# Performance work log

Hardware: AMD Instinct MI355X
Metric: run time of the kernel (lower is better)

## Reference

```python
import jax, jax.numpy as jnp
import numpy as np

H = 512; VT = 10000; VN = 1000; ET = 256; EN = 256
A = 50; B = 8; L = 128; SOS = 0


def setup_inputs():
    key = jax.random.key(0)
    ks = jax.random.split(key, 12)
    g = lambda k, s: jax.random.normal(k, s, jnp.float32) * 0.02
    inp = {}
    inp["n_tensor"] = jax.random.randint(ks[0], (B, L), 0, VN)
    inp["t_tensor"] = jax.random.randint(ks[1], (B, L), 0, VT)
    inp["p_tensor"] = jax.random.randint(ks[2], (B, L), 0, L)
    # embedding tables; padding rows (padding_idx) zeroed as nn.Embedding init does
    inp["embN"] = g(ks[3], (VN, EN)).at[VN - 1].set(0.0)
    inp["embT"] = g(ks[4], (VT + A + 3, ET)).at[VT - 1].set(0.0)
    inp["W_hid"] = g(ks[5], (H, H)); inp["b_hid"] = jnp.zeros((H,), jnp.float32)
    inp["W_mem"] = g(ks[6], (H, H)); inp["b_mem"] = jnp.zeros((H,), jnp.float32)
    inp["v_w"] = g(ks[7], (H,)); inp["v_b"] = jnp.zeros((), jnp.float32)
    inp["W_ih"] = g(ks[8], (4 * H, EN + ET)); inp["W_hh"] = g(ks[9], (4 * H, H))
    inp["b_ih"] = jnp.zeros((4 * H,), jnp.float32); inp["b_hh"] = jnp.zeros((4 * H,), jnp.float32)
    inp["W_g"] = g(ks[10], (3 * H, VT + 3)); inp["b_g"] = jnp.zeros((VT + 3,), jnp.float32)
    inp["W_s"] = g(ks[11], (2 * H,)); inp["b_s"] = jnp.zeros((), jnp.float32)
    return inp


def _forward(embN, embT, W_hid, b_hid, W_mem, b_mem, v_w, v_b,
             W_ih, W_hh, b_ih, b_hh, W_g, b_g, W_s, b_s,
             n_tensor, t_tensor, p_tensor):
    full_mask = (n_tensor == VN - 1)                      # [B, L] eof mask
    sos = jnp.full((B, 1), SOS, n_tensor.dtype)
    n_in = jnp.concatenate([sos, n_tensor[:, :-1]], 1)    # teacher-forced inputs
    t_in = jnp.concatenate([sos, t_tensor[:, :-1]], 1)
    par = jnp.concatenate([jnp.zeros((B, 1), p_tensor.dtype), p_tensor[:, :-1]], 1)
    hs0 = jnp.zeros((B, L, H), jnp.float32)               # growing memory buffer
    h0 = jnp.zeros((B, H), jnp.float32)
    c0 = jnp.zeros((B, H), jnp.float32)
    barange = jnp.arange(B)
    arangeA = jnp.arange(A)

    def step(carry, xs):
        hs, h, c = carry
        t, n_t, t_t, p_t, tgt = xs
        # embedding gathers + single-layer LSTM cell (torch gate order i,f,g,o)
        x = jnp.concatenate([embN[n_t], embT[t_t]], 1)    # [B, EN+ET]
        gates = x @ W_ih.T + h @ W_hh.T + (b_ih + b_hh)
        i, f, gg, o = jnp.split(gates, 4, axis=1)
        c = jax.nn.sigmoid(f) * c + jax.nn.sigmoid(i) * jnp.tanh(gg)
        h = jax.nn.sigmoid(o) * jnp.tanh(c)
        # sliding-window memory hs[:, max(t-A,0):t], fixed-size slice + validity mask
        s = jnp.maximum(t - A, 0)
        mem = jax.lax.dynamic_slice(hs, (0, s, 0), (B, A, H))   # [B, A, H]
        fm = jax.lax.dynamic_slice(full_mask, (0, s), (B, A))   # [B, A]
        valid = (s + arangeA) < t                               # [A] positions already written
        mask = fm | ~valid[None, :]
        # additive attention: v^T tanh(W_hid h + W_mem mem)
        sc = jnp.tanh((h @ W_hid.T + b_hid)[:, None, :] + mem @ W_mem.T + b_mem)
        sc = sc @ v_w + v_b                                     # [B, A]
        sc = jnp.where(mask, -1e20, sc)
        attn = jax.nn.softmax(sc, axis=1)
        context = jnp.einsum('ba,bah->bh', attn, mem)
        h_parent = hs[barange, p_t]                             # per-batch gather on memory
        wt = jax.nn.log_softmax(jnp.concatenate([context, h, h_parent], 1) @ W_g + b_g, axis=1)
        log_attn = jax.nn.log_softmax(sc, axis=1)
        st = jax.nn.log_sigmoid(jnp.concatenate([context, h], 1) @ W_s + b_s)[:, None]  # [B,1]
        out = jnp.concatenate(
            [st + wt, jnp.log(jnp.clip(-jnp.expm1(st), 1e-18, 1e18)) + log_attn], 1)    # [B, VT+3+A]
        hs = hs.at[:, t].set(h)                                 # scatter new hidden into buffer
        loss_t = -jnp.take_along_axis(out, tgt[:, None], axis=1)[:, 0]  # NLLLoss(reduction='none')
        pred = jnp.argmax(out, axis=1)
        return (hs, h, c), (loss_t, pred)

    ts = jnp.arange(L)
    _, (losses, preds) = jax.lax.scan(
        step, (hs0, h0, c0), (ts, n_in.T, t_in.T, par.T, t_tensor.T))
    return losses.sum(), preds.T


def reference(n_tensor, t_tensor, p_tensor, embN, embT, W_hid, b_hid, W_mem, b_mem,
              v_w, v_b, W_ih, W_hh, b_ih, b_hh, W_g, b_g, W_s, b_s):
    return _forward(embN, embT, W_hid, b_hid, W_mem, b_mem, v_w, v_b,
                    W_ih, W_hh, b_ih, b_hh, W_g, b_g, W_s, b_s,
                    n_tensor, t_tensor, p_tensor)
```

## Files before the change

kernel.cpp:

```cpp
#include <hip/hip_runtime.h>
#include <hip/hip_bf16.h>
#include <math.h>

#define H_ 512
#define VN_ 1000
#define NG_ 10003
#define NGP_ 10240
#define NCHUNK 80
#define A_ 50
#define B_ 8
#define L_ 128
#define R_ 1024

typedef __hip_bfloat16 bf16;
typedef __attribute__((ext_vector_type(8))) short bf16x8;
typedef __attribute__((ext_vector_type(4))) float f32x4;

typedef union { unsigned long long u[2]; bf16x8 v; } frag_u;

__device__ __forceinline__ float fsig(float x) { return 1.0f / (1.0f + __expf(-x)); }
__device__ __forceinline__ float ftanh(float x) { return 1.0f - 2.0f / (1.0f + __expf(2.0f * x)); }

__device__ __forceinline__ short b16(float v) {
    __hip_bfloat16 h = __float2bfloat16(v);
    return *(short*)&h;
}

__device__ __forceinline__ unsigned long long ald(const unsigned long long* p) {
    return __hip_atomic_load(p, __ATOMIC_RELAXED, __HIP_MEMORY_SCOPE_AGENT);
}
__device__ __forceinline__ int aldi(const int* p) {
    return __hip_atomic_load(p, __ATOMIC_RELAXED, __HIP_MEMORY_SCOPE_AGENT);
}
__device__ __forceinline__ void ast32(unsigned int* p, unsigned int v) {
    __hip_atomic_store(p, v, __ATOMIC_RELAXED, __HIP_MEMORY_SCOPE_AGENT);
}
__device__ __forceinline__ void asti(int* p, int v) {
    __hip_atomic_store(p, v, __ATOMIC_RELAXED, __HIP_MEMORY_SCOPE_AGENT);
}

__global__ void k_prep(int* flags, float* bkq,
                       const float* __restrict__ bmem, const float* __restrict__ bhid,
                       float* out,
                       const float* __restrict__ Wih, bf16* __restrict__ wihb,
                       const int* __restrict__ nt, const int* __restrict__ tt,
                       const float* __restrict__ embN, const float* __restrict__ embT,
                       bf16* __restrict__ X)
{
    const int i = blockIdx.x * 256 + threadIdx.x;
    const int total = gridDim.x * 256;
    if (i < 32)
        __hip_atomic_store(&flags[i], 0, __ATOMIC_RELAXED, __HIP_MEMORY_SCOPE_AGENT);
    if (i < 1024) bkq[i] = (i < 512) ? bmem[i] : bhid[i - 512];
    if (i == 0) out[0] = 0.f;
    for (int j = i; j < 2048 * 512; j += total)
        wihb[j] = __float2bfloat16(Wih[j]);
    {
        int r = i >> 9, k = i & 511;
        int t = r >> 3, b = r & 7;
        float v;
        if (k < 256) {
            int id = (t == 0) ? 0 : nt[b * L_ + t - 1];
            v = embN[id * 256 + k];
        } else {
            int id = (t == 0) ? 0 : tt[b * L_ + t - 1];
            v = embT[id * 256 + (k - 256)];
        }
        X[i] = __float2bfloat16(v);
    }
}

#define LSTM_BLOCKS 16
#define XTRA 240

#define DECLW(i) bf16x8 Wa##i, Wb##i;
#define LOADW(i) { \
    float4 a0 = *(const float4*)(wr0 + (i)*32); \
    float4 a1 = *(const float4*)(wr0 + (i)*32 + 4); \
    float4 c0 = *(const float4*)(wr1 + (i)*32); \
    float4 c1 = *(const float4*)(wr1 + (i)*32 + 4); \
    Wa##i[0]=b16(a0.x); Wa##i[1]=b16(a0.y); Wa##i[2]=b16(a0.z); Wa##i[3]=b16(a0.w); \
    Wa##i[4]=b16(a1.x); Wa##i[5]=b16(a1.y); Wa##i[6]=b16(a1.z); Wa##i[7]=b16(a1.w); \
    Wb##i[0]=b16(c0.x); Wb##i[1]=b16(c0.y); Wb##i[2]=b16(c0.z); Wb##i[3]=b16(c0.w); \
    Wb##i[4]=b16(c1.x); Wb##i[5]=b16(c1.y); Wb##i[6]=b16(c1.z); Wb##i[7]=b16(c1.w); }
#define LDF(i) frag_u fu##i; fu##i.u[0] = ald(src + (i)*128); fu##i.u[1] = ald(src + (i)*128 + 1);
#define MM(i) \
    acc0 = __builtin_amdgcn_mfma_f32_16x16x32_bf16(Wa##i, fu##i.v, acc0, 0, 0, 0); \
    acc1 = __builtin_amdgcn_mfma_f32_16x16x32_bf16(Wb##i, fu##i.v, acc1, 0, 0, 0);

__launch_bounds__(256, 1)
__global__ void k_lstm(const float* __restrict__ Whh, const float* __restrict__ xg,
                       bf16* __restrict__ hsb,
                       unsigned long long* __restrict__ bfr, int* __restrict__ flags,
                       const float* __restrict__ Wg, bf16* __restrict__ WT,
                       const float* __restrict__ Wmem, const float* __restrict__ Whid,
                       bf16* __restrict__ wkq)
{
    __shared__ float gl[4][32][9];
    __shared__ short S[64][65];
    const int tid  = threadIdx.x;
    const int x    = blockIdx.x;

    if (x >= LSTM_BLOCKS) {
        for (int i = (x - LSTM_BLOCKS) * 256 + tid; i < 2 * 512 * 512; i += XTRA * 256) {
            float v = (i < 512 * 512) ? Wmem[i] : Whid[i - 512 * 512];
            wkq[i] = __float2bfloat16(v);
        }
        const int c = tid & 63;
        const int r0 = (tid >> 6) * 16;
        const int n_l = tid >> 2;
        const int kq = (tid & 3) * 16;
        for (int tile = x - LSTM_BLOCKS; tile < 160 * 24; tile += XTRA) {
            int n0 = (tile % 160) * 64, k0 = (tile / 160) * 64;
            __syncthreads();
            #pragma unroll
            for (int i = 0; i < 16; ++i) {
                int k = r0 + i;
                int n = n0 + c;
                float v = (n < NG_) ? Wg[(size_t)(k0 + k) * NG_ + n] : 0.f;
                S[c][k] = b16(v);
            }
            __syncthreads();
            bf16* dst = WT + (size_t)(n0 + n_l) * 1536 + k0 + kq;
            #pragma unroll
            for (int j = 0; j < 2; ++j) {
                bf16x8 v;
                #pragma unroll
                for (int e = 0; e < 8; ++e) v[e] = S[n_l][kq + j * 8 + e];
                *(bf16x8*)(dst + j * 8) = v;
            }
        }
        return;
    }

    const int lane = tid & 63;
    const int w    = tid >> 6;
    const int m_l  = lane & 15;
    const int kg   = lane >> 4;
    const int n    = lane & 15;
    unsigned int* bfr32 = (unsigned int*)bfr;

    const float* wr0 = Whh + (size_t)(w * 512 + x * 32 + m_l) * 512 + kg * 8;
    const float* wr1 = wr0 + (size_t)16 * 512;
    DECLW(0)  DECLW(1)  DECLW(2)  DECLW(3)  DECLW(4)  DECLW(5)  DECLW(6)  DECLW(7)
    DECLW(8)  DECLW(9)  DECLW(10) DECLW(11) DECLW(12) DECLW(13) DECLW(14) DECLW(15)
    LOADW(0)  LOADW(1)  LOADW(2)  LOADW(3)  LOADW(4)  LOADW(5)  LOADW(6)  LOADW(7)
    LOADW(8)  LOADW(9)  LOADW(10) LOADW(11) LOADW(12) LOADW(13) LOADW(14) LOADW(15)
    asm volatile("" : "+v"(Wa0), "+v"(Wb0), "+v"(Wa1), "+v"(Wb1), "+v"(Wa2), "+v"(Wb2),
                      "+v"(Wa3), "+v"(Wb3), "+v"(Wa4), "+v"(Wb4), "+v"(Wa5), "+v"(Wb5),
                      "+v"(Wa6), "+v"(Wb6), "+v"(Wa7), "+v"(Wb7));
    asm volatile("" : "+v"(Wa8), "+v"(Wb8), "+v"(Wa9), "+v"(Wb9), "+v"(Wa10), "+v"(Wb10),
                      "+v"(Wa11), "+v"(Wb11), "+v"(Wa12), "+v"(Wb12), "+v"(Wa13), "+v"(Wb13),
                      "+v"(Wa14), "+v"(Wb14), "+v"(Wa15), "+v"(Wb15));

    const int u_l = tid >> 3;
    const int b   = tid & 7;
    float creg = 0.f;
    int fearly = 0;

    for (int t = 0; t < L_; ++t) {
        const float* xr = xg + ((size_t)t * B_ + b) * 2048 + x * 32 + u_l;
        float xi = xr[0], xf = xr[512], xgg = xr[1024], xo = xr[1536];

        f32x4 acc0 = {0.f, 0.f, 0.f, 0.f};
        f32x4 acc1 = {0.f, 0.f, 0.f, 0.f};
        if (t > 0) {
            if (!__all(fearly >= t)) {
                for (;;) {
                    int v = (lane < LSTM_BLOCKS) ? aldi(&flags[lane]) : t;
                    if (__all(v >= t)) break;
                    __builtin_amdgcn_s_sleep(1);
                }
            }
            const unsigned long long* src =
                bfr + (size_t)((t + 1) & 1) * 2048 + lane * 2;
            LDF(0)  LDF(1)  LDF(2)  LDF(3)  LDF(4)  LDF(5)  LDF(6)  LDF(7)
            LDF(8)  LDF(9)  LDF(10) LDF(11) LDF(12) LDF(13) LDF(14) LDF(15)
            __builtin_amdgcn_sched_barrier(0);
            MM(0)  MM(1)  MM(2)  MM(3)  MM(4)  MM(5)  MM(6)  MM(7)
            MM(8)  MM(9)  MM(10) MM(11) MM(12) MM(13) MM(14) MM(15)
        }
        if (n < 8) {
            #pragma unroll
            for (int i = 0; i < 4; ++i) {
                gl[w][kg * 4 + i][n]      = acc0[i];
                gl[w][16 + kg * 4 + i][n] = acc1[i];
            }
        }
        __syncthreads();
        float gi = gl[0][u_l][b] + xi;
        float gf = gl[1][u_l][b] + xf;
        float gg = gl[2][u_l][b] + xgg;
        float go = gl[3][u_l][b] + xo;
        float iv = fsig(gi), fv = fsig(gf), gv = ftanh(gg), ov = fsig(go);
        creg = fv * creg + iv * gv;
        float h = ov * ftanh(creg);
        float h2 = __shfl_xor(h, 8);
        unsigned pay = 0;
        if ((u_l & 1) == 0) {
            pay = (unsigned)(unsigned short)b16(h)
                | ((unsigned)(unsigned short)b16(h2) << 16);
            int q = u_l >> 3, p = (u_l & 7) >> 1;
            ast32(bfr32 + (size_t)(t & 1) * 4096 + x * 256 + (b + 16 * q) * 4 + p, pay);
        }
        fearly = (lane < LSTM_BLOCKS && lane != x) ? aldi(&flags[lane]) : 0x7FFFFFFF;
        asm volatile("s_waitcnt vmcnt(0)" ::: "memory");
        __syncthreads();
        if (tid == 0)
            asti(&flags[x], t + 1);
        if ((u_l & 1) == 0)
            *(unsigned int*)(hsb + (size_t)(t * B_ + b) * 512 + x * 32 + u_l) = pay;
    }
}

__launch_bounds__(256)
__global__ void k_attn(const bf16* __restrict__ hsb, const float* __restrict__ kmq,
                       const float* __restrict__ vw,
                       const float* __restrict__ vb, const int* __restrict__ nt,
                       const int* __restrict__ pt, const float* __restrict__ Wsv,
                       const float* __restrict__ bs, bf16* __restrict__ gcat,
                       float* __restrict__ logattn, float* __restrict__ stbuf)
{
    const int r = blockIdx.x;
    const int t = r >> 3, b = r & 7;
    const int tid = threadIdx.x;
    const int lane = tid & 63, wave = tid >> 6;
    int s = t - A_; if (s < 0) s = 0;
    __shared__ float qv[512];
    __shared__ float vwl[512];
    __shared__ float sc[A_];
    __shared__ float attn[A_];
    __shared__ float red[4];
    for (int i = tid; i < 512; i += 256) {
        qv[i] = kmq[(size_t)r * 1024 + 512 + i];
        vwl[i] = vw[i];
    }
    __syncthreads();
    for (int a = wave; a < A_; a += 4) {
        int pos = s + a;
        float v = -1e20f;
        bool masked = (pos >= t) || (nt[b * L_ + pos] == VN_ - 1);
        if (!masked) {
            const float* kr = kmq + (size_t)(pos * B_ + b) * 1024;
            float p = 0.f;
            for (int k = lane; k < 512; k += 64)
                p += vwl[k] * ftanh(qv[k] + kr[k]);
            for (int off = 32; off; off >>= 1) p += __shfl_down(p, off);
            v = p + vb[0];
        }
        if (lane == 0) sc[a] = v;
    }
    __syncthreads();
    if (tid < 64) {
        float v = (tid < A_) ? sc[tid] : -INFINITY;
        float m = v;
        for (int off = 32; off; off >>= 1) m = fmaxf(m, __shfl_xor(m, off));
        float e = (tid < A_) ? expf(v - m) : 0.f;
        float d = e;
        for (int off = 32; off; off >>= 1) d += __shfl_xor(d, off);
        if (tid < A_) {
            attn[tid] = e / d;
            logattn[(size_t)r * A_ + tid] = (v - m) - logf(d);
        }
    }
    __syncthreads();
    const int k0 = tid * 2;
    float c0 = 0.f, c1 = 0.f;
    for (int a = 0; a < A_; ++a) {
        int pos = s + a;
        if (pos >= t) break;
        float w = attn[a];
        unsigned u = *(const unsigned*)((const unsigned short*)hsb + (size_t)(pos * B_ + b) * 512 + k0);
        c0 += w * __uint_as_float(u << 16);
        c1 += w * __uint_as_float(u & 0xffff0000u);
    }
    unsigned ucur = *(const unsigned*)((const unsigned short*)hsb + (size_t)(t * B_ + b) * 512 + k0);
    int par = (t == 0) ? 0 : pt[b * L_ + t - 1];
    unsigned upar = 0;
    if (par < t)
        upar = *(const unsigned*)((const unsigned short*)hsb + (size_t)(par * B_ + b) * 512 + k0);
    float hx = __uint_as_float(ucur << 16), hy = __uint_as_float(ucur & 0xffff0000u);
    bf16* g = gcat + (size_t)r * 1536;
    g[k0]     = __float2bfloat16(c0);
    g[k0 + 1] = __float2bfloat16(c1);
    *(unsigned*)(g + 512 + k0)  = ucur;
    *(unsigned*)(g + 1024 + k0) = upar;
    float part = c0 * Wsv[k0] + c1 * Wsv[k0 + 1]
               + hx * Wsv[512 + k0] + hy * Wsv[512 + k0 + 1];
    for (int off = 32; off; off >>= 1) part += __shfl_down(part, off);
    if (lane == 0) red[wave] = part;
    __syncthreads();
    if (tid == 0) {
        float z = red[0] + red[1] + red[2] + red[3] + bs[0];
        stbuf[r] = -log1pf(expf(-z));
    }
}

__launch_bounds__(256, 2)
__global__ void k_gemm128b(const bf16* __restrict__ Ag, const bf16* __restrict__ Bg,
                           const float* __restrict__ b1, const float* __restrict__ b2,
                           float* __restrict__ C, int N, int K)
{
    __shared__ short As[128 * 32];
    __shared__ short Bs[128 * 32];
    const int tid = threadIdx.x;
    const int lane = tid & 63, wave = tid >> 6;
    const int wr = wave >> 1, wc = wave & 1;
    const int m0 = blockIdx.y * 128, n0 = blockIdx.x * 128;
    f32x4 acc[4][4] = {};
    for (int k0 = 0; k0 < K; k0 += 32) {
        __syncthreads();
        #pragma unroll
        for (int h = 0; h < 2; ++h) {
            int o = tid + h * 256;
            int row = o >> 2;
            int kc = (o & 3) ^ (row & 3);
            const bf16* ga = Ag + (size_t)(m0 + row) * K + k0 + kc * 8;
            const bf16* gb = Bg + (size_t)(n0 + row) * K + k0 + kc * 8;
            unsigned ldso = h * 4096 + wave * 1024;
            __builtin_amdgcn_global_load_lds(
                (const __attribute__((address_space(1))) void*)ga,
                (__attribute__((address_space(3))) void*)((char*)As + ldso), 16, 0, 0);
            __builtin_amdgcn_global_load_lds(
                (const __attribute__((address_space(1))) void*)gb,
                (__attribute__((address_space(3))) void*)((char*)Bs + ldso), 16, 0, 0);
        }
        asm volatile("s_waitcnt vmcnt(0)" ::: "memory");
        __syncthreads();
        bf16x8 af[4], bf[4];
        #pragma unroll
        for (int mi = 0; mi < 4; ++mi) {
            int ra = wr * 64 + mi * 16 + (lane & 15);
            af[mi] = *(const bf16x8*)&As[ra * 32 + (((lane >> 4) ^ (ra & 3)) * 8)];
        }
        #pragma unroll
        for (int ni = 0; ni < 4; ++ni) {
            int rb = wc * 64 + ni * 16 + (lane & 15);
            bf[ni] = *(const bf16x8*)&Bs[rb * 32 + (((lane >> 4) ^ (rb & 3)) * 8)];
        }
        #pragma unroll
        for (int mi = 0; mi < 4; ++mi)
            #pragma unroll
            for (int ni = 0; ni < 4; ++ni)
                acc[mi][ni] = __builtin_amdgcn_mfma_f32_16x16x32_bf16(af[mi], bf[ni], acc[mi][ni], 0, 0, 0);
    }
    const int col = lane & 15, rq = (lane >> 4) * 4;
    #pragma unroll
    for (int mi = 0; mi < 4; ++mi)
        #pragma unroll
        for (int ni = 0; ni < 4; ++ni) {
            int nn = n0 + wc * 64 + ni * 16 + col;
            float bias = (b1 ? b1[nn] : 0.f) + (b2 ? b2[nn] : 0.f);
            #pragma unroll
            for (int i = 0; i < 4; ++i)
                C[(size_t)(m0 + wr * 64 + mi * 16 + rq + i) * N + nn] = acc[mi][ni][i] + bias;
        }
}

__launch_bounds__(256, 2)
__global__ void k_gemm128p(const bf16* __restrict__ Ag, const bf16* __restrict__ Bg,
                           const float* __restrict__ bg, const int* __restrict__ tt,
                           float* __restrict__ pst)
{
    __shared__ short As[128 * 32];
    __shared__ short Bs[128 * 32];
    __shared__ float bgl[128];
    __shared__ float mrg[128][6];
    const int tid = threadIdx.x;
    const int lane = tid & 63, wave = tid >> 6;
    const int wr = wave >> 1, wc = wave & 1;
    const int col16 = lane & 15, rq = (lane >> 4) * 4;
    const int chunk = blockIdx.x;
    const int m0 = blockIdx.y * 128;
    const int n0 = chunk * 128;
    const int K = 1536;

    if (tid < 128) bgl[tid] = (n0 + tid < NG_) ? bg[n0 + tid] : -INFINITY;

    float M[4][4], S[4][4], AV[4][4], TGT[4][4]; int AI[4][4]; int tgt[4][4];
    #pragma unroll
    for (int mi = 0; mi < 4; ++mi)
        #pragma unroll
        for (int i = 0; i < 4; ++i) {
            M[mi][i] = -INFINITY; S[mi][i] = 0.f; AV[mi][i] = -INFINITY;
            TGT[mi][i] = -INFINITY; AI[mi][i] = 0x7FFFFFFF;
            int row = m0 + wr * 64 + mi * 16 + rq + i;
            tgt[mi][i] = tt[(row & 7) * L_ + (row >> 3)];
        }

    f32x4 acc[4][4] = {};
    for (int k0 = 0; k0 < K; k0 += 32) {
        __syncthreads();
        #pragma unroll
        for (int h = 0; h < 2; ++h) {
            int o = tid + h * 256;
            int row = o >> 2;
            int kc = (o & 3) ^ (row & 3);
            const bf16* ga = Ag + (size_t)(m0 + row) * K + k0 + kc * 8;
            const bf16* gb = Bg + (size_t)(n0 + row) * K + k0 + kc * 8;
            unsigned ldso = h * 4096 + wave * 1024;
            __builtin_amdgcn_global_load_lds(
                (const __attribute__((address_space(1))) void*)ga,
                (__attribute__((address_space(3))) void*)((char*)As + ldso), 16, 0, 0);
            __builtin_amdgcn_global_load_lds(
                (const __attribute__((address_space(1))) void*)gb,
                (__attribute__((address_space(3))) void*)((char*)Bs + ldso), 16, 0, 0);
        }
        asm volatile("s_waitcnt vmcnt(0)" ::: "memory");
        __syncthreads();
        bf16x8 af[4], bf[4];
        #pragma unroll
        for (int mi = 0; mi < 4; ++mi) {
            int ra = wr * 64 + mi * 16 + col16;
            af[mi] = *(const bf16x8*)&As[ra * 32 + (((lane >> 4) ^ (ra & 3)) * 8)];
        }
        #pragma unroll
        for (int ni = 0; ni < 4; ++ni) {
            int rb = wc * 64 + ni * 16 + col16;
            bf[ni] = *(const bf16x8*)&Bs[rb * 32 + (((lane >> 4) ^ (rb & 3)) * 8)];
        }
        #pragma unroll
        for (int mi = 0; mi < 4; ++mi)
            #pragma unroll
            for (int ni = 0; ni < 4; ++ni)
                acc[mi][ni] = __builtin_amdgcn_mfma_f32_16x16x32_bf16(af[mi], bf[ni], acc[mi][ni], 0, 0, 0);
    }
    #pragma unroll
    for (int mi = 0; mi < 4; ++mi)
        #pragma unroll
        for (int i = 0; i < 4; ++i) {
            float v[4]; int nn[4];
            #pragma unroll
            for (int ni = 0; ni < 4; ++ni) {
                int cl = wc * 64 + ni * 16 + col16;
                v[ni] = acc[mi][ni][i] + bgl[cl];
                nn[ni] = n0 + cl;
            }
            float lv = v[0]; int li = nn[0];
            #pragma unroll
            for (int ni = 1; ni < 4; ++ni)
                if (v[ni] > lv) { lv = v[ni]; li = nn[ni]; }
            #pragma unroll
            for (int off = 1; off < 16; off <<= 1) {
                float ov = __shfl_xor(lv, off); int oi = __shfl_xor(li, off);
                if (ov > lv || (ov == lv && oi < li)) { lv = ov; li = oi; }
            }
            float nM = lv;
            float add = 0.f;
            if (nM != -INFINITY) {
                #pragma unroll
                for (int ni = 0; ni < 4; ++ni) add += expf(v[ni] - nM);
                #pragma unroll
                for (int off = 1; off < 16; off <<= 1) add += __shfl_xor(add, off);
            }
            M[mi][i] = nM; S[mi][i] = add;
            AV[mi][i] = lv; AI[mi][i] = li;
            float tv = -INFINITY;
            #pragma unroll
            for (int ni = 0; ni < 4; ++ni)
                if (nn[ni] == tgt[mi][i]) tv = v[ni];
            #pragma unroll
            for (int off = 1; off < 16; off <<= 1)
                tv = fmaxf(tv, __shfl_xor(tv, off));
            TGT[mi][i] = tv;
        }
    __syncthreads();
    if (wc == 1 && col16 == 0) {
        #pragma unroll
        for (int mi = 0; mi < 4; ++mi)
            #pragma unroll
            for (int i = 0; i < 4; ++i) {
                int rl = wr * 64 + mi * 16 + rq + i;
                mrg[rl][0] = M[mi][i]; mrg[rl][1] = S[mi][i];
                mrg[rl][2] = AV[mi][i]; mrg[rl][3] = __int_as_float(AI[mi][i]);
                mrg[rl][4] = TGT[mi][i];
            }
    }
    __syncthreads();
    if (wc == 0 && col16 == 0) {
        #pragma unroll
        for (int mi = 0; mi < 4; ++mi)
            #pragma unroll
            for (int i = 0; i < 4; ++i) {
                int rl = wr * 64 + mi * 16 + rq + i;
                float oM = mrg[rl][0], oS = mrg[rl][1], oAV = mrg[rl][2];
                int oAI = __float_as_int(mrg[rl][3]);
                float oT = mrg[rl][4];
                float nM = fmaxf(M[mi][i], oM);
                float s1 = (S[mi][i] > 0.f) ? S[mi][i] * expf(M[mi][i] - nM) : 0.f;
                float s2 = (oS > 0.f) ? oS * expf(oM - nM) : 0.f;
                float av = AV[mi][i]; int ai = AI[mi][i];
                if (oAV > av || (oAV == av && oAI < ai)) { av = oAV; ai = oAI; }
                float* p = pst + ((size_t)chunk * R_ + (m0 + rl)) * 8;
                p[0] = nM; p[1] = s1 + s2; p[2] = av;
                p[3] = __int_as_float(ai); p[4] = fmaxf(TGT[mi][i], oT);
            }
    }
}

__launch_bounds__(64)
__global__ void k_loss2(const float* __restrict__ pst, const float* __restrict__ logattn,
                        const float* __restrict__ stbuf, float* __restrict__ out)
{
    const int r = blockIdx.x;
    const int lane = threadIdx.x;
    float M = -INFINITY, S = 0.f, AV = -INFINITY, TGT = -INFINITY;
    int AI = 0x7FFFFFFF;
    for (int c = lane; c < NCHUNK; c += 64) {
        const float* p = pst + ((size_t)c * R_ + r) * 8;
        float oM = p[0], oS = p[1], oAV = p[2];
        int oAI = __float_as_int(p[3]);
        float oT = p[4];
        float nM = fmaxf(M, oM);
        float s1 = (S > 0.f) ? S * expf(M - nM) : 0.f;
        float s2 = (oS > 0.f) ? oS * expf(oM - nM) : 0.f;
        M = nM; S = s1 + s2;
        if (oAV > AV || (oAV == AV && oAI < AI)) { AV = oAV; AI = oAI; }
        TGT = fmaxf(TGT, oT);
    }
    for (int off = 32; off; off >>= 1) {
        float oM = __shfl_xor(M, off), oS = __shfl_xor(S, off);
        float oAV = __shfl_xor(AV, off), oT = __shfl_xor(TGT, off);
        int oAI = __shfl_xor(AI, off);
        float nM = fmaxf(M, oM);
        float s1 = (S > 0.f) ? S * expf(M - nM) : 0.f;
        float s2 = (oS > 0.f) ? oS * expf(oM - nM) : 0.f;
        M = nM; S = s1 + s2;
        if (oAV > AV || (oAV == AV && oAI < AI)) { AV = oAV; AI = oAI; }
        TGT = fmaxf(TGT, oT);
    }
    if (lane == 0) {
        float lse = M + logf(S);
        float st = stbuf[r];
        const float* la = logattn + (size_t)r * A_;
        float lamax = la[0]; int aidx = 0;
        for (int a = 1; a < A_; ++a) if (la[a] > lamax) { lamax = la[a]; aidx = a; }
        float e1 = -expm1f(st);
        e1 = fminf(fmaxf(e1, 1e-18f), 1e18f);
        float lm = logf(e1);
        float p1 = st + M - lse;
        float p2 = lm + lamax;
        int pred = (p1 >= p2) ? AI : (NG_ + aidx);
        float loss = -(st + TGT - lse);
        atomicAdd(&out[0], loss);
        int t = r >> 3, b = r & 7;
        out[1 + b * L_ + t] = (float)pred;
    }
}

extern "C" void kernel_launch(void* const* d_in, const int* in_sizes, int n_in,
                              void* d_out, int out_size, void* d_ws, size_t ws_size,
                              hipStream_t stream)
{
    (void)in_sizes; (void)n_in; (void)out_size; (void)ws_size;
    const int*   nt    = (const int*)d_in[0];
    const int*   tt    = (const int*)d_in[1];
    const int*   pt    = (const int*)d_in[2];
    const float* embN  = (const float*)d_in[3];
    const float* embT  = (const float*)d_in[4];
    const float* W_hid = (const float*)d_in[5];
    const float* b_hid = (const float*)d_in[6];
    const float* W_mem = (const float*)d_in[7];
    const float* b_mem = (const float*)d_in[8];
    const float* v_w   = (const float*)d_in[9];
    const float* v_b   = (const float*)d_in[10];
    const float* W_ih  = (const float*)d_in[11];
    const float* W_hh  = (const float*)d_in[12];
    const float* b_ih  = (const float*)d_in[13];
    const float* b_hh  = (const float*)d_in[14];
    const float* W_g   = (const float*)d_in[15];
    const float* b_g   = (const float*)d_in[16];
    const float* W_s   = (const float*)d_in[17];
    const float* b_s   = (const float*)d_in[18];
    float* out = (float*)d_out;

    char* ws = (char*)d_ws;
    size_t o = 0;
    bf16*  WGT  = (bf16*)(ws + o);  o += (size_t)NGP_ * 1536 * 2;
    float* XG   = (float*)(ws + o); o += (size_t)R_ * 2048 * 4;
    bf16*  HSB  = (bf16*)(ws + o);  o += (size_t)R_ * H_ * 2;
    float* KMQ  = (float*)(ws + o); o += (size_t)R_ * 1024 * 4;
    bf16*  WKQ  = (bf16*)(ws + o);  o += (size_t)1024 * 512 * 2;
    float* BKQ  = (float*)(ws + o); o += (size_t)1024 * 4;
    bf16*  XB   = (bf16*)(ws + o);  o += (size_t)R_ * H_ * 2;
    bf16*  WIHB = (bf16*)(ws + o);  o += (size_t)2048 * 512 * 2;
    bf16*  GC   = (bf16*)(ws + o);  o += (size_t)R_ * 1536 * 2;
    float* LA   = (float*)(ws + o); o += (size_t)R_ * A_ * 4;
    float* ST   = (float*)(ws + o); o += (size_t)R_ * 4;
    float* PST  = (float*)(ws + o); o += (size_t)NCHUNK * R_ * 8 * 4;
    unsigned long long* BFR = (unsigned long long*)(ws + o); o += (size_t)4096 * 8;
    int*   FLG  = (int*)(ws + o);   o += 256;

    k_prep<<<2048, 256, 0, stream>>>(FLG, BKQ, b_mem, b_hid, out,
                                     W_ih, WIHB, nt, tt, embN, embT, XB);
    k_gemm128b<<<dim3(2048 / 128, R_ / 128), 256, 0, stream>>>(XB, WIHB, b_ih, b_hh, XG, 2048, 512);
    k_lstm<<<LSTM_BLOCKS + XTRA, 256, 0, stream>>>(W_hh, XG, HSB, BFR, FLG,
                                                   W_g, WGT, W_mem, W_hid, WKQ);
    k_gemm128b<<<dim3(1024 / 128, R_ / 128), 256, 0, stream>>>(HSB, WKQ, BKQ, nullptr, KMQ, 1024, 512);
    k_attn<<<R_, 256, 0, stream>>>(HSB, KMQ, v_w, v_b, nt, pt, W_s, b_s, GC, LA, ST);
    k_gemm128p<<<dim3(NCHUNK, R_ / 128), 256, 0, stream>>>(GC, WGT, b_g, tt, PST);
    k_loss2<<<R_, 64, 0, stream>>>(PST, LA, ST, out);
}
```

Before: 563.4 us.

## Fuse input-projection GEMM into LSTM kernel with per-chunk readiness flags

Removes the separate x@W_ih GEMM launch and computes it inside the persistent LSTM kernel's extra blocks. Each 128-row chunk publishes a completion counter, so the recurrent blocks can start once the first chunk is ready and wait only when they reach a later chunk. The MFMA accumulation over K is also split into two independent accumulator chains to shorten the dependency chain. This adds flag polling and atomic loads of XG, and it gives the weight-conversion work in those blocks less throughput.

```diff
diff --git a/kernel.cpp b/kernel.cpp
--- a/kernel.cpp
+++ b/kernel.cpp
@@ -32,10 +32,16 @@
 __device__ __forceinline__ int aldi(const int* p) {
     return __hip_atomic_load(p, __ATOMIC_RELAXED, __HIP_MEMORY_SCOPE_AGENT);
 }
+__device__ __forceinline__ float aldf(const float* p) {
+    return __hip_atomic_load(p, __ATOMIC_RELAXED, __HIP_MEMORY_SCOPE_AGENT);
+}
 __device__ __forceinline__ void ast32(unsigned int* p, unsigned int v) {
     __hip_atomic_store(p, v, __ATOMIC_RELAXED, __HIP_MEMORY_SCOPE_AGENT);
 }
 __device__ __forceinline__ void asti(int* p, int v) {
+    __hip_atomic_store(p, v, __ATOMIC_RELAXED, __HIP_MEMORY_SCOPE_AGENT);
+}
+__device__ __forceinline__ void astf(float* p, float v) {
     __hip_atomic_store(p, v, __ATOMIC_RELAXED, __HIP_MEMORY_SCOPE_AGENT);
 }
 
@@ -84,25 +90,94 @@
     Wb##i[0]=b16(c0.x); Wb##i[1]=b16(c0.y); Wb##i[2]=b16(c0.z); Wb##i[3]=b16(c0.w); \
     Wb##i[4]=b16(c1.x); Wb##i[5]=b16(c1.y); Wb##i[6]=b16(c1.z); Wb##i[7]=b16(c1.w); }
 #define LDF(i) frag_u fu##i; fu##i.u[0] = ald(src + (i)*128); fu##i.u[1] = ald(src + (i)*128 + 1);
-#define MM(i) \
-    acc0 = __builtin_amdgcn_mfma_f32_16x16x32_bf16(Wa##i, fu##i.v, acc0, 0, 0, 0); \
-    acc1 = __builtin_amdgcn_mfma_f32_16x16x32_bf16(Wb##i, fu##i.v, acc1, 0, 0, 0);
+#define MMa(i) \
+    acc0a = __builtin_amdgcn_mfma_f32_16x16x32_bf16(Wa##i, fu##i.v, acc0a, 0, 0, 0); \
+    acc1a = __builtin_amdgcn_mfma_f32_16x16x32_bf16(Wb##i, fu##i.v, acc1a, 0, 0, 0);
+#define MMb(i) \
+    acc0b = __builtin_amdgcn_mfma_f32_16x16x32_bf16(Wa##i, fu##i.v, acc0b, 0, 0, 0); \
+    acc1b = __builtin_amdgcn_mfma_f32_16x16x32_bf16(Wb##i, fu##i.v, acc1b, 0, 0, 0);
 
 __launch_bounds__(256, 1)
-__global__ void k_lstm(const float* __restrict__ Whh, const float* __restrict__ xg,
+__global__ void k_lstm(const float* __restrict__ Whh, float* __restrict__ xg,
                        bf16* __restrict__ hsb,
                        unsigned long long* __restrict__ bfr, int* __restrict__ flags,
                        const float* __restrict__ Wg, bf16* __restrict__ WT,
                        const float* __restrict__ Wmem, const float* __restrict__ Whid,
-                       bf16* __restrict__ wkq)
+                       bf16* __restrict__ wkq,
+                       const bf16* __restrict__ xb, const bf16* __restrict__ wihb,
+                       const float* __restrict__ bih, const float* __restrict__ bhh)
 {
     __shared__ float gl[4][32][9];
     __shared__ short S[64][65];
+    __shared__ short As[128 * 32];
+    __shared__ short Bs[128 * 32];
     const int tid  = threadIdx.x;
     const int x    = blockIdx.x;
+    const int lane = tid & 63;
+    const int wave = tid >> 6;
 
     if (x >= LSTM_BLOCKS) {
-        for (int i = (x - LSTM_BLOCKS) * 256 + tid; i < 2 * 512 * 512; i += XTRA * 256) {
+        const int d = x - LSTM_BLOCKS;
+        if (d < 128) {
+            const int m0 = (d >> 4) * 128, n0g = (d & 15) * 128;
+            const int wr = wave >> 1, wc = wave & 1;
+            const int K = 512;
+            f32x4 acc[4][4] = {};
+            for (int k0 = 0; k0 < K; k0 += 32) {
+                __syncthreads();
+                #pragma unroll
+                for (int h = 0; h < 2; ++h) {
+                    int o = tid + h * 256;
+                    int row = o >> 2;
+                    int kc = (o & 3) ^ (row & 3);
+                    const bf16* ga = xb + (size_t)(m0 + row) * K + k0 + kc * 8;
+                    const bf16* gb = wihb + (size_t)(n0g + row) * K + k0 + kc * 8;
+                    unsigned ldso = h * 4096 + wave * 1024;
+                    __builtin_amdgcn_global_load_lds(
+                        (const __attribute__((address_space(1))) void*)ga,
+                        (__attribute__((address_space(3))) void*)((char*)As + ldso), 16, 0, 0);
+                    __builtin_amdgcn_global_load_lds(
+                        (const __attribute__((address_space(1))) void*)gb,
+                        (__attribute__((address_space(3))) void*)((char*)Bs + ldso), 16, 0, 0);
+                }
+                asm volatile("s_waitcnt vmcnt(0)" ::: "memory");
+                __syncthreads();
+                bf16x8 af[4], bfv[4];
+                #pragma unroll
+                for (int mi = 0; mi < 4; ++mi) {
+                    int ra = wr * 64 + mi * 16 + (lane & 15);
+                    af[mi] = *(const bf16x8*)&As[ra * 32 + (((lane >> 4) ^ (ra & 3)) * 8)];
+                }
+                #pragma unroll
+                for (int ni = 0; ni < 4; ++ni) {
+                    int rb = wc * 64 + ni * 16 + (lane & 15);
+                    bfv[ni] = *(const bf16x8*)&Bs[rb * 32 + (((lane >> 4) ^ (rb & 3)) * 8)];
+                }
+                #pragma unroll
+                for (int mi = 0; mi < 4; ++mi)
+                    #pragma unroll
+                    for (int ni = 0; ni < 4; ++ni)
+                        acc[mi][ni] = __builtin_amdgcn_mfma_f32_16x16x32_bf16(af[mi], bfv[ni], acc[mi][ni], 0, 0, 0);
+            }
+            const int col = lane & 15, rq = (lane >> 4) * 4;
+            #pragma unroll
+            for (int mi = 0; mi < 4; ++mi)
+                #pragma unroll
+                for (int ni = 0; ni < 4; ++ni) {
+                    int nn = n0g + wc * 64 + ni * 16 + col;
+                    float bias = bih[nn] + bhh[nn];
+                    #pragma unroll
+                    for (int i = 0; i < 4; ++i)
+                        astf(xg + (size_t)(m0 + wr * 64 + mi * 16 + rq + i) * 2048 + nn,
+                             acc[mi][ni][i] + bias);
+                }
+            asm volatile("s_waitcnt vmcnt(0)" ::: "memory");
+            __syncthreads();
+            if (tid == 0)
+                __hip_atomic_fetch_add(&flags[16 + (d >> 4)], 1,
+                                       __ATOMIC_RELAXED, __HIP_MEMORY_SCOPE_AGENT);
+        }
+        for (int i = d * 256 + tid; i < 2 * 512 * 512; i += XTRA * 256) {
             float v = (i < 512 * 512) ? Wmem[i] : Whid[i - 512 * 512];
             wkq[i] = __float2bfloat16(v);
         }
@@ -110,7 +185,7 @@
         const int r0 = (tid >> 6) * 16;
         const int n_l = tid >> 2;
         const int kq = (tid & 3) * 16;
-        for (int tile = x - LSTM_BLOCKS; tile < 160 * 24; tile += XTRA) {
+        for (int tile = d; tile < 160 * 24; tile += XTRA) {
             int n0 = (tile % 160) * 64, k0 = (tile / 160) * 64;
             __syncthreads();
             #pragma unroll
@@ -133,8 +208,7 @@
         return;
     }
 
-    const int lane = tid & 63;
-    const int w    = tid >> 6;
+    const int w    = wave;
     const int m_l  = lane & 15;
     const int kg   = lane >> 4;
     const int n    = lane & 15;
@@ -157,29 +231,46 @@
     const int b   = tid & 7;
     float creg = 0.f;
     int fearly = 0;
+    int xgconf = 0;
+
+    for (;;) {
+        int v = (lane == 0) ? aldi(&flags[16]) : 16;
+        if (__all(v >= 16)) break;
+        __builtin_amdgcn_s_sleep(8);
+    }
 
     for (int t = 0; t < L_; ++t) {
-        const float* xr = xg + ((size_t)t * B_ + b) * 2048 + x * 32 + u_l;
-        float xi = xr[0], xf = xr[512], xgg = xr[1024], xo = xr[1536];
-
-        f32x4 acc0 = {0.f, 0.f, 0.f, 0.f};
-        f32x4 acc1 = {0.f, 0.f, 0.f, 0.f};
+        const int chunk = t >> 4;
+        f32x4 acc0a = {0.f, 0.f, 0.f, 0.f}, acc0b = {0.f, 0.f, 0.f, 0.f};
+        f32x4 acc1a = {0.f, 0.f, 0.f, 0.f}, acc1b = {0.f, 0.f, 0.f, 0.f};
         if (t > 0) {
-            if (!__all(fearly >= t)) {
+            if (!__all(fearly >= t) || chunk > xgconf) {
                 for (;;) {
-                    int v = (lane < LSTM_BLOCKS) ? aldi(&flags[lane]) : t;
+                    int v;
+                    if (lane < 16) v = aldi(&flags[lane]);
+                    else if (lane == 16 && chunk > xgconf)
+                        v = (aldi(&flags[16 + chunk]) >= 16) ? t : t - 1;
+                    else v = t;
                     if (__all(v >= t)) break;
                     __builtin_amdgcn_s_sleep(1);
                 }
-            }
+                xgconf = chunk;
+            }
+        }
+        const float* xr = xg + ((size_t)t * B_ + b) * 2048 + x * 32 + u_l;
+        float xi = aldf(xr), xf = aldf(xr + 512), xgg = aldf(xr + 1024), xo = aldf(xr + 1536);
+
+        if (t > 0) {
             const unsigned long long* src =
                 bfr + (size_t)((t + 1) & 1) * 2048 + lane * 2;
             LDF(0)  LDF(1)  LDF(2)  LDF(3)  LDF(4)  LDF(5)  LDF(6)  LDF(7)
             LDF(8)  LDF(9)  LDF(10) LDF(11) LDF(12) LDF(13) LDF(14) LDF(15)
             __builtin_amdgcn_sched_barrier(0);
-            MM(0)  MM(1)  MM(2)  MM(3)  MM(4)  MM(5)  MM(6)  MM(7)
-            MM(8)  MM(9)  MM(10) MM(11) MM(12) MM(13) MM(14) MM(15)
-        }
+            MMa(0)  MMa(1)  MMa(2)  MMa(3)  MMa(4)  MMa(5)  MMa(6)  MMa(7)
+            MMb(8)  MMb(9)  MMb(10) MMb(11) MMb(12) MMb(13) MMb(14) MMb(15)
+        }
+        f32x4 acc0 = acc0a + acc0b;
+        f32x4 acc1 = acc1a + acc1b;
         if (n < 8) {
             #pragma unroll
             for (int i = 0; i < 4; ++i) {
@@ -593,9 +684,9 @@
 
     k_prep<<<2048, 256, 0, stream>>>(FLG, BKQ, b_mem, b_hid, out,
                                      W_ih, WIHB, nt, tt, embN, embT, XB);
-    k_gemm128b<<<dim3(2048 / 128, R_ / 128), 256, 0, stream>>>(XB, WIHB, b_ih, b_hh, XG, 2048, 512);
     k_lstm<<<LSTM_BLOCKS + XTRA, 256, 0, stream>>>(W_hh, XG, HSB, BFR, FLG,
-                                                   W_g, WGT, W_mem, W_hid, WKQ);
+                                                   W_g, WGT, W_mem, W_hid, WKQ,
+                                                   XB, WIHB, b_ih, b_hh);
     k_gemm128b<<<dim3(1024 / 128, R_ / 128), 256, 0, stream>>>(HSB, WKQ, BKQ, nullptr, KMQ, 1024, 512);
     k_attn<<<R_, 256, 0, stream>>>(HSB, KMQ, v_w, v_b, nt, pt, W_s, b_s, GC, LA, ST);
     k_gemm128p<<<dim3(NCHUNK, R_ / 128), 256, 0, stream>>>(GC, WGT, b_g, tt, PST);
```

New measurement: 592.8 us. 1.05x slower.
